# Optimization experiments

Hardware: AMD Instinct MI355X
Metric: run time of the kernel (lower is better)

The kernel has to match this reference:

```python
import jax, jax.numpy as jnp
import numpy as np

B, CIN, COUT, T, H, W, NH = 8, 16, 16, 32, 16, 16, 4
DIN = CIN * H * W    # 4096
DOUT = COUT * H * W  # 4096
DH = DOUT // NH      # 1024


def conv3d(x, w, b, pad):
    y = jax.lax.conv_general_dilated(
        x, w, window_strides=(1, 1, 1), padding=((pad, pad),) * 3,
        dimension_numbers=('NCDHW', 'OIDHW', 'NCDHW'))
    return y + b[None, :, None, None, None]


def instance_norm(x, eps=1e-5):
    # InstanceNorm3d default: no affine, normalize per (B,C) over (T,H,W)
    mu = x.mean(axis=(2, 3, 4), keepdims=True)
    var = ((x - mu) ** 2).mean(axis=(2, 3, 4), keepdims=True)
    return (x - mu) * jax.lax.rsqrt(var + eps)


def slstm(x, Wg, bg, Rg):
    # x: (B,T,D). Wg: (4,D,D) input weights [i,f,z,o]; bg: (4,D);
    # Rg: (NH,4,DH,DH) block-diagonal per-head recurrent weights.
    Bb, Tt, D = x.shape
    Gx = jnp.einsum('btd,god->btgo', x, Wg) + bg  # (B,T,4,D)

    def step(carry, gx):
        h, c, n, m = carry
        hh = h.reshape(Bb, NH, DH)
        gh = jnp.einsum('bhd,hgod->bhgo', hh, Rg)          # (B,NH,4,DH)
        pre = gx + gh.transpose(0, 2, 1, 3).reshape(Bb, 4, D)
        i_pre, f_pre, z_pre, o_pre = pre[:, 0], pre[:, 1], pre[:, 2], pre[:, 3]
        # stabilized exponential gating (xLSTM sLSTM)
        m_new = jnp.maximum(f_pre + m, i_pre)
        i = jnp.exp(i_pre - m_new)
        f = jnp.exp(f_pre + m - m_new)
        c = f * c + i * jnp.tanh(z_pre)
        n = f * n + i
        h = jax.nn.sigmoid(o_pre) * c / n
        return (h, c, n, m_new), h

    init = tuple(jnp.zeros((Bb, D), x.dtype) for _ in range(4))
    _, hs = jax.lax.scan(step, init, Gx.transpose(1, 0, 2, 3))  # hs: (T,B,D)
    return hs.transpose(1, 0, 2)


def setup_inputs():
    key = jax.random.key(0)
    ks = jax.random.split(key, 8)
    s = 0.02
    return {
        'x': jax.random.normal(ks[0], (B, CIN, T, H, W), jnp.float32),
        'c1_w': jax.random.normal(ks[1], (COUT, CIN, 3, 3, 3), jnp.float32) * 0.05,
        'c1_b': jnp.zeros((COUT,), jnp.float32),
        'c2_w': jax.random.normal(ks[2], (COUT, COUT, 3, 3, 3), jnp.float32) * 0.05,
        'c2_b': jnp.zeros((COUT,), jnp.float32),
        'c3_w': jax.random.normal(ks[3], (COUT, COUT, 3, 3, 3), jnp.float32) * 0.05,
        'c3_b': jnp.zeros((COUT,), jnp.float32),
        'pre_w': jax.random.normal(ks[4], (DOUT, DIN), jnp.float32) * s,
        'pre_b': jnp.zeros((DOUT,), jnp.float32),
        'lstm_W': jax.random.normal(ks[5], (4, DOUT, DOUT), jnp.float32) * s,
        'lstm_b': jnp.zeros((4, DOUT), jnp.float32),
        'lstm_R': jax.random.normal(ks[6], (NH, 4, DH, DH), jnp.float32) * s,
        'attn_w': jax.random.normal(ks[7], (1, 2 * COUT), jnp.float32) * 0.05,
        'attn_b': jnp.zeros((1,), jnp.float32),
    }


def reference(x, c1_w, c1_b, c2_w, c2_b, c3_w, c3_b, pre_w, pre_b,
              lstm_W, lstm_b, lstm_R, attn_w, attn_b):
    # conv3d branch: conv -> IN -> relu -> conv -> relu -> conv -> relu
    y = jax.nn.relu(instance_norm(conv3d(x, c1_w, c1_b, 1)))
    y = jax.nn.relu(conv3d(y, c2_w, c2_b, 1))
    out3d = jax.nn.relu(conv3d(y, c3_w, c3_b, 1))
    # sLSTM branch
    xs = x.transpose(0, 2, 1, 3, 4).reshape(B, T, DIN)
    xs = xs @ pre_w.T + pre_b
    hs = slstm(xs, lstm_W, lstm_b, lstm_R)                 # (B,T,DOUT)
    s_out = hs.reshape(B, T, COUT, H, W).transpose(0, 2, 1, 3, 4)
    # attention-gated fusion: cat -> 1x1x1 conv -> sigmoid -> weighted sum
    comb = jnp.concatenate([s_out, out3d], axis=1)         # (B,2*COUT,T,H,W)
    alpha = jax.nn.sigmoid(jnp.einsum('bcthw,oc->bothw', comb, attn_w)
                           + attn_b[None, :, None, None, None])
    return alpha * out3d + (1 - alpha) * s_out
```

## Files before the change

kernel.cpp:

```cpp
#include <hip/hip_runtime.h>
#include <hip/hip_bf16.h>
#include <cstddef>

#define BB   8
#define CIN  16
#define COUT 16
#define TT   32
#define HH   16
#define WW   16
#define DIN  4096
#define DOUT 4096
#define NH   4
#define DH   1024
#define SPAT 8192
#define NSEQ 256

typedef __attribute__((ext_vector_type(8))) short  bf16x8;
typedef __attribute__((ext_vector_type(4))) float  f32x4;
typedef __attribute__((ext_vector_type(4))) unsigned short us4;
typedef __attribute__((ext_vector_type(4))) int    i32x4;
typedef unsigned short ushort_t;
typedef unsigned long long u64_t;

static __device__ __forceinline__ ushort_t f2bf(float f) {
    union { float f; unsigned u; } v; v.f = f;
    unsigned r = (v.u + 0x7fffu + ((v.u >> 16) & 1u)) >> 16;
    return (ushort_t)r;
}
static __device__ __forceinline__ float bf2f(ushort_t u) {
    union { unsigned u; float f; } v; v.u = ((unsigned)u) << 16;
    return v.f;
}

__global__ void setup_kernel(const float* __restrict__ x, ushort_t* __restrict__ xt,
                             const float* __restrict__ w1, const float* __restrict__ w2,
                             const float* __restrict__ w3,
                             float* __restrict__ cw1, float* __restrict__ cw2,
                             float* __restrict__ cw3, int* __restrict__ flags) {
    int bid = blockIdx.x;
    if (bid < 1024) {
        int idx = bid * 256 + threadIdx.x;
        int n = idx >> 10, k4 = (idx & 1023) * 4;
        int b = n >> 5, t = n & 31, c = k4 >> 8, hw = k4 & 255;
        f32x4 f = *(const f32x4*)&x[(((size_t)(b * CIN + c) * TT + t)) * 256 + hw];
        us4 o;
        #pragma unroll
        for (int i = 0; i < 4; ++i) o[i] = f2bf(f[i]);
        *(us4*)&xt[(size_t)n * DIN + k4] = o;
    } else if (bid < 1105) {
        int i = (bid - 1024) * 256 + threadIdx.x;
        if (i < 3 * 6912) {
            int set = i / 6912, j = i - set * 6912;
            const float* w = (set == 0) ? w1 : (set == 1) ? w2 : w3;
            float* cw      = (set == 0) ? cw1 : (set == 1) ? cw2 : cw3;
            int o = j & 15, r = j >> 4;
            int k = r % 27, ci = r / 27;
            cw[j] = w[(size_t)(o * CIN + ci) * 27 + k];
        }
    } else {
        int j = (bid - 1105) * 256 + threadIdx.x;
        ((i32x4*)flags)[j] = (i32x4){0, 0, 0, 0};
    }
}

template<int BN, int BK, bool OUT_BF16, bool ADD_BIAS>
__device__ __forceinline__
void gemm_body(char* smem, int bx, int by, int nsplit,
               const ushort_t* __restrict__ A, const float* __restrict__ B,
               const float* __restrict__ bias, void* __restrict__ C,
               int N, int K) {
    constexpr int NF  = BN / 16;
    constexpr int TPR = 256 / BN;
    constexpr int FPT = BK / TPR;
    ushort_t* Al = (ushort_t*)smem;
    ushort_t* Bl = Al + 2 * 256 * BK;
    int tid  = threadIdx.x;
    int lane = tid & 63;
    int wv   = tid >> 6;
    int n0 = bx * BN;
    int ksp = K / nsplit;
    int kS  = by * ksp;

    f32x4 acc[4][NF];
    #pragma unroll
    for (int i = 0; i < 4; ++i)
        #pragma unroll
        for (int j = 0; j < NF; ++j) acc[i][j] = (f32x4){0.f, 0.f, 0.f, 0.f};

    auto stageA = [&](int buf, int k0) {
        #pragma unroll
        for (int q = 0; q < 8; ++q) {
            int rbase = wv * 64 + q * 8;
            int row = rbase + (lane >> 3);
            const ushort_t* g = A + (size_t)row * K + k0 + (lane & 7) * 8;
            __builtin_amdgcn_global_load_lds(
                (const __attribute__((address_space(1))) void*)g,
                (__attribute__((address_space(3))) void*)&Al[(buf * 256 + rbase) * BK],
                16, 0, 0);
        }
    };
    auto stageB = [&](int buf, int k0) {
        int r  = tid / TPR;
        int cs = (tid % TPR) * FPT;
        const float* g = B + (size_t)(n0 + r) * K + k0 + cs;
        #pragma unroll
        for (int q = 0; q < FPT / 4; ++q) {
            f32x4 f = *(const f32x4*)(g + q * 4);
            us4 pk;
            #pragma unroll
            for (int e = 0; e < 4; ++e) pk[e] = f2bf(f[e]);
            *(us4*)&Bl[(buf * BN + r) * BK + cs + q * 4] = pk;
        }
    };
    auto compute = [&](int buf) {
        #pragma unroll
        for (int ks = 0; ks < BK / 32; ++ks) {
            bf16x8 af[4], bfr[NF];
            #pragma unroll
            for (int i = 0; i < 4; ++i)
                af[i] = *(const bf16x8*)&Al[(buf * 256 + wv * 64 + i * 16 + (lane & 15)) * BK + ks * 32 + (lane >> 4) * 8];
            #pragma unroll
            for (int j = 0; j < NF; ++j)
                bfr[j] = *(const bf16x8*)&Bl[(buf * BN + j * 16 + (lane & 15)) * BK + ks * 32 + (lane >> 4) * 8];
            #pragma unroll
            for (int i = 0; i < 4; ++i)
                #pragma unroll
                for (int j = 0; j < NF; ++j)
                    acc[i][j] = __builtin_amdgcn_mfma_f32_16x16x32_bf16(af[i], bfr[j], acc[i][j], 0, 0, 0);
        }
    };

    stageA(0, kS); stageB(0, kS);
    __syncthreads();
    int nk = ksp / BK;
    int cur = 0;
    for (int t = 0; t < nk; ++t) {
        if (t + 1 < nk) { stageA(cur ^ 1, kS + (t + 1) * BK); stageB(cur ^ 1, kS + (t + 1) * BK); }
        compute(cur);
        __syncthreads();
        cur ^= 1;
    }

    size_t cofs = (size_t)by * 256 * N;
    #pragma unroll
    for (int i = 0; i < 4; ++i) {
        int row = wv * 64 + i * 16 + (lane >> 4) * 4;
        #pragma unroll
        for (int j = 0; j < NF; ++j) {
            int col = n0 + j * 16 + (lane & 15);
            float bv = ADD_BIAS ? bias[col] : 0.f;
            #pragma unroll
            for (int r = 0; r < 4; ++r) {
                float v = acc[i][j][r] + bv;
                if constexpr (OUT_BF16) ((ushort_t*)C)[cofs + (size_t)(row + r) * N + col] = f2bf(v);
                else                    ((float*)C)[cofs + (size_t)(row + r) * N + col] = v;
            }
        }
    }
}

template<bool NORM, bool PSUM>
__device__ __forceinline__
void conv_body(char* smem, int blk,
               const float* __restrict__ in, const float* __restrict__ cw,
               const float* __restrict__ bias, const float* __restrict__ stats,
               float* __restrict__ out, float* __restrict__ psum, int relu) {
    float* xin = (float*)smem;
    int b = blk >> 6, t = (blk >> 1) & 31, half = blk & 1;
    int tid = threadIdx.x;

    for (int i = tid; i < CIN * 3 * 256; i += 256) {
        int hw = i & 255, r = i >> 8;
        int kt = r % 3, ci = r / 3;
        int tt = t + kt - 1;
        float v = 0.f;
        if ((unsigned)tt < TT) {
            v = in[((size_t)(b * CIN + ci) * TT + tt) * 256 + hw];
            if constexpr (NORM) {
                float mu = stats[(b * CIN + ci) * 2];
                float rs = stats[(b * CIN + ci) * 2 + 1];
                v = fmaxf((v - mu) * rs, 0.f);
            }
        }
        xin[(ci * 3 + kt) * 256 + hw] = v;
    }
    __syncthreads();

    int h = tid >> 4, wx = tid & 15;
    f32x4 a0 = *(const f32x4*)&bias[half * 8];
    f32x4 a1 = *(const f32x4*)&bias[half * 8 + 4];

    for (int ci = 0; ci < CIN; ++ci) {
        #pragma unroll
        for (int kt = 0; kt < 3; ++kt) {
            #pragma unroll
            for (int kh = 0; kh < 3; ++kh) {
                int h2 = h + kh - 1;
                bool vh = (unsigned)h2 < HH;
                int h2c = vh ? h2 : 0;
                #pragma unroll
                for (int kw = 0; kw < 3; ++kw) {
                    int w2 = wx + kw - 1;
                    bool v = vh && ((unsigned)w2 < WW);
                    int w2c = ((unsigned)w2 < WW) ? w2 : 0;
                    float xv = xin[(ci * 3 + kt) * 256 + h2c * 16 + w2c];
                    xv = v ? xv : 0.f;
                    const float* wp = cw + (size_t)(ci * 27 + kt * 9 + kh * 3 + kw) * 16 + half * 8;
                    f32x4 w0 = *(const f32x4*)(wp);
                    f32x4 w1 = *(const f32x4*)(wp + 4);
                    a0 += xv * w0; a1 += xv * w1;
                }
            }
        }
    }
    float accs[8];
    #pragma unroll
    for (int i = 0; i < 4; ++i) { accs[i] = a0[i]; accs[4 + i] = a1[i]; }
    #pragma unroll
    for (int o = 0; o < 8; ++o) {
        float v = accs[o];
        if (relu) v = fmaxf(v, 0.f);
        out[((size_t)(b * COUT + half * 8 + o) * TT + t) * 256 + tid] = v;
    }

    if constexpr (PSUM) {
        __syncthreads();
        float* sm = xin;
        int wv = tid >> 6;
        #pragma unroll
        for (int o = 0; o < 8; ++o) {
            float s = accs[o];
            float q = accs[o] * accs[o];
            #pragma unroll
            for (int m = 1; m < 64; m <<= 1) {
                s += __shfl_xor(s, m, 64);
                q += __shfl_xor(q, m, 64);
            }
            if ((tid & 63) == 0) { sm[wv * 16 + o * 2] = s; sm[wv * 16 + o * 2 + 1] = q; }
        }
        __syncthreads();
        if (tid < 16) {
            int o = tid >> 1, which = tid & 1;
            float v = sm[o * 2 + which] + sm[16 + o * 2 + which]
                    + sm[32 + o * 2 + which] + sm[48 + o * 2 + which];
            psum[((((size_t)(b * 32 + t) * 2 + half) * 8 + o) * 2) + which] = v;
        }
    }
}

__global__ __launch_bounds__(256, 2)
void fused1_kernel(const ushort_t* __restrict__ xt, const float* __restrict__ pre_w,
                   const float* __restrict__ pre_b, ushort_t* __restrict__ xs2b,
                   const float* __restrict__ x, const float* __restrict__ cw1,
                   const float* __restrict__ c1_b, float* __restrict__ y1,
                   float* __restrict__ psum) {
    extern __shared__ char smem[];
    if (blockIdx.x < 256)
        gemm_body<16, 64, true, true>(smem, blockIdx.x, 0, 1, xt, pre_w, pre_b, xs2b, DOUT, DIN);
    else
        conv_body<false, true>(smem, blockIdx.x - 256, x, cw1, c1_b, nullptr, y1, psum, 0);
}

__global__ __launch_bounds__(256, 2)
void fused2_kernel(const ushort_t* __restrict__ xs2b, const float* __restrict__ lstm_W,
                   float* __restrict__ Gx,
                   const float* __restrict__ y1, const float* __restrict__ cw2,
                   const float* __restrict__ c2_b, const float* __restrict__ stats,
                   float* __restrict__ y2) {
    extern __shared__ char smem[];
    if (blockIdx.x < 1024)
        gemm_body<32, 64, false, false>(smem, blockIdx.x & 511, blockIdx.x >> 9, 2,
                                        xs2b, lstm_W, nullptr, Gx, 4 * DOUT, DOUT);
    else
        conv_body<true, false>(smem, blockIdx.x - 1024, y1, cw2, c2_b, stats, y2, nullptr, 1);
}

__global__ __launch_bounds__(256, 2)
void conv3_kernel(const float* __restrict__ y2, const float* __restrict__ cw3,
                  const float* __restrict__ c3_b, float* __restrict__ out3d) {
    extern __shared__ char smem[];
    conv_body<false, false>(smem, blockIdx.x, y2, cw3, c3_b, nullptr, out3d, nullptr, 1);
}

__global__ void inorm_stats_kernel(const float* __restrict__ psum, float* __restrict__ stats) {
    int tid = threadIdx.x;
    if (tid < 128) {
        int b = tid >> 4, c = tid & 15;
        int half = c >> 3, ch = c & 7;
        float sum = 0.f, sq = 0.f;
        for (int t = 0; t < TT; ++t) {
            size_t base = (((size_t)(b * 32 + t) * 2 + half) * 8 + ch) * 2;
            sum += psum[base];
            sq  += psum[base + 1];
        }
        float mu = sum / (float)SPAT;
        float var = sq / (float)SPAT - mu * mu;
        stats[(b * CIN + c) * 2]     = mu;
        stats[(b * CIN + c) * 2 + 1] = rsqrtf(var + 1e-5f);
    }
}

#define GXPS ((size_t)NSEQ * 4 * DOUT)

__global__ __launch_bounds__(256, 1)
void lstm_persist_kernel(const float* __restrict__ R,
                         const float* __restrict__ Gx,
                         const float* __restrict__ lstm_b,
                         unsigned* __restrict__ hfr,
                         int* __restrict__ flags) {
    __shared__ ushort_t Rl[4][32][64 * 8];
    __shared__ float gh_p[4][4][16][8];

    int tid  = threadIdx.x;
    int lane = tid & 63;
    int w    = tid >> 6;
    int head = blockIdx.x >> 6;
    int oc   = blockIdx.x & 63;

    #pragma unroll 4
    for (int n = 0; n < 64; ++n) {
        int g = n >> 4, r = n & 15;
        const float* src = R + ((size_t)((head * 4 + g) * DH + oc * 16 + r)) * DH + tid * 4;
        f32x4 f = *(const f32x4*)src;
        int k0 = tid * 4;
        int ks = k0 >> 5;
        int kI = (k0 >> 3) & 3;
        int e8 = k0 & 7;
        union { ushort_t u[4]; u64_t q; } pk;
        #pragma unroll
        for (int e = 0; e < 4; ++e) pk.u[e] = f2bf(f[e]);
        *(u64_t*)&Rl[g][ks][((kI << 4) | r) * 8 + e8] = pk.q;
    }

    int arow = lane & 15;
    int part = arow >> 3;
    int bb   = arow & 7;
    int kseg = lane >> 4;

    int gb  = tid >> 4;
    int gol = tid & 15;
    int gd  = head * DH + oc * 16 + gol;
    int o_h = oc * 16 + gol;
    unsigned hslot = ((unsigned)head * 32 + (o_h >> 5)) * 256 + gb * 32 + (o_h & 31);
    float c_r = 0.f, n_r = 0.f, m_r = 0.f;
    float lb0 = 0.f, lb1 = 0.f, lb2 = 0.f, lb3 = 0.f;
    if (tid < 128) {
        lb0 = lstm_b[gd];
        lb1 = lstm_b[DOUT + gd];
        lb2 = lstm_b[2 * DOUT + gd];
        lb3 = lstm_b[3 * DOUT + gd];
    }

    __syncthreads();

    for (int t = 0; t < TT; ++t) {
        float gx0 = lb0, gx1 = lb1, gx2 = lb2, gx3 = lb3;
        if (tid < 128) {
            size_t gxoff = ((size_t)(gb * TT + t)) * (4 * DOUT) + gd;
            #pragma unroll
            for (int p = 0; p < 2; ++p) {
                const float* gp = Gx + p * GXPS + gxoff;
                gx0 += gp[0];
                gx1 += gp[DOUT];
                gx2 += gp[2 * DOUT];
                gx3 += gp[3 * DOUT];
            }
        }

        if (t > 0) {
            const int* fl = flags + (((t - 1) * 4 + head) << 6);
            for (;;) {
                int v = __hip_atomic_load(fl + lane, __ATOMIC_RELAXED,
                                          __HIP_MEMORY_SCOPE_AGENT);
                if (__all(v != 0)) break;
                __builtin_amdgcn_s_sleep(1);
            }

            const u64_t* hb = (const u64_t*)hfr
                + ((((size_t)(t - 1) * 4 + head) * 32) * 256 + bb * 32 + kseg * 8) / 2;
            bf16x8 hf[8];
            #pragma unroll
            for (int j = 0; j < 8; ++j) {
                const u64_t* p = hb + (size_t)(w * 8 + j) * 128;
                union { ushort_t u[8]; bf16x8 v; } fr;
                #pragma unroll
                for (int e2 = 0; e2 < 4; ++e2) {
                    u64_t q = __hip_atomic_load(p + e2, __ATOMIC_RELAXED,
                                                __HIP_MEMORY_SCOPE_AGENT);
                    unsigned q0 = (unsigned)q, q1 = (unsigned)(q >> 32);
                    fr.u[e2 * 2]     = part ? (ushort_t)(q0 >> 16) : (ushort_t)(q0 & 0xffffu);
                    fr.u[e2 * 2 + 1] = part ? (ushort_t)(q1 >> 16) : (ushort_t)(q1 & 0xffffu);
                }
                hf[j] = fr.v;
            }

            f32x4 acc[4];
            #pragma unroll
            for (int g = 0; g < 4; ++g) acc[g] = (f32x4){0.f, 0.f, 0.f, 0.f};
            #pragma unroll
            for (int g = 0; g < 4; ++g)
                #pragma unroll
                for (int j = 0; j < 8; ++j) {
                    bf16x8 a = *(const bf16x8*)&Rl[g][w * 8 + j][lane * 8];
                    acc[g] = __builtin_amdgcn_mfma_f32_16x16x32_bf16(a, hf[j], acc[g], 0, 0, 0);
                }
            #pragma unroll
            for (int g = 0; g < 4; ++g)
                #pragma unroll
                for (int r = 0; r < 4; ++r)
                    acc[g][r] += __shfl_xor(acc[g][r], 8, 64);
            if (part == 0) {
                int orow0 = kseg * 4;
                #pragma unroll
                for (int g = 0; g < 4; ++g)
                    #pragma unroll
                    for (int r = 0; r < 4; ++r)
                        gh_p[w][g][orow0 + r][bb] = acc[g][r];
            }
        } else {
            for (int i = tid; i < 4 * 4 * 16 * 8; i += 256)
                ((float*)gh_p)[i] = 0.f;
        }
        __syncthreads();

        if (tid < 128) {
            float ip = gx0 +
                gh_p[0][0][gol][gb] + gh_p[1][0][gol][gb] + gh_p[2][0][gol][gb] + gh_p[3][0][gol][gb];
            float fp = gx1 +
                gh_p[0][1][gol][gb] + gh_p[1][1][gol][gb] + gh_p[2][1][gol][gb] + gh_p[3][1][gol][gb];
            float zp = gx2 +
                gh_p[0][2][gol][gb] + gh_p[1][2][gol][gb] + gh_p[2][2][gol][gb] + gh_p[3][2][gol][gb];
            float op = gx3 +
                gh_p[0][3][gol][gb] + gh_p[1][3][gol][gb] + gh_p[2][3][gol][gb] + gh_p[3][3][gol][gb];
            float mn = fmaxf(fp + m_r, ip);
            float iv = __expf(ip - mn);
            float fv = __expf(fp + m_r - mn);
            float zc = fminf(fmaxf(zp, -9.f), 9.f);
            float th = 1.f - 2.f / (__expf(2.f * zc) + 1.f);
            c_r = fv * c_r + iv * th;
            n_r = fv * n_r + iv;
            float sig = 1.f / (1.f + __expf(-op));
            float hv = sig * c_r / n_r;
            m_r = mn;
            unsigned hi = f2bf(hv);
            unsigned lo = f2bf(hv - bf2f((ushort_t)hi));
            __hip_atomic_store(&hfr[(size_t)t * 32768 + hslot],
                               hi | (lo << 16),
                               __ATOMIC_RELAXED, __HIP_MEMORY_SCOPE_AGENT);
        }
        __syncthreads();
        if (tid == 0)
            __hip_atomic_store(&flags[((t * 4 + head) << 6) + oc], 1,
                               __ATOMIC_RELAXED, __HIP_MEMORY_SCOPE_AGENT);
    }
}

__global__ void combine_kernel(const unsigned* __restrict__ hfr,
                               const float* __restrict__ out3d,
                               const float* __restrict__ attn_w,
                               const float* __restrict__ attn_b,
                               float* __restrict__ out) {
    int idx = blockIdx.x * 256 + threadIdx.x;
    int hw = idx & 255;
    int t  = (idx >> 8) & 31;
    int b  = idx >> 13;
    float dot = attn_b[0];
    float sv[16], ov[16];
    #pragma unroll
    for (int ch = 0; ch < 16; ++ch) {
        int d = ch * 256 + hw;
        int head = d >> 10, o_h = d & 1023;
        size_t slot = (size_t)t * 32768 + (size_t)head * 8192
                    + (o_h >> 5) * 256 + b * 32 + (o_h & 31);
        unsigned v32 = hfr[slot];
        float s = bf2f((ushort_t)(v32 & 0xffffu)) + bf2f((ushort_t)(v32 >> 16));
        float o3 = out3d[(((size_t)(b * COUT + ch) * TT + t)) * 256 + hw];
        sv[ch] = s; ov[ch] = o3;
        dot += attn_w[ch] * s + attn_w[16 + ch] * o3;
    }
    float alpha = 1.f / (1.f + expf(-dot));
    #pragma unroll
    for (int ch = 0; ch < 16; ++ch) {
        out[(((size_t)(b * COUT + ch) * TT + t)) * 256 + hw] =
            alpha * ov[ch] + (1.f - alpha) * sv[ch];
    }
}

extern "C" void kernel_launch(void* const* d_in, const int* in_sizes, int n_in,
                              void* d_out, int out_size, void* d_ws, size_t ws_size,
                              hipStream_t stream) {
    const float* x      = (const float*)d_in[0];
    const float* c1_w   = (const float*)d_in[1];
    const float* c1_b   = (const float*)d_in[2];
    const float* c2_w   = (const float*)d_in[3];
    const float* c2_b   = (const float*)d_in[4];
    const float* c3_w   = (const float*)d_in[5];
    const float* c3_b   = (const float*)d_in[6];
    const float* pre_w  = (const float*)d_in[7];
    const float* pre_b  = (const float*)d_in[8];
    const float* lstm_W = (const float*)d_in[9];
    const float* lstm_b = (const float*)d_in[10];
    const float* lstm_R = (const float*)d_in[11];
    const float* attn_w = (const float*)d_in[12];
    const float* attn_b = (const float*)d_in[13];
    float* out = (float*)d_out;

    float* wsf = (float*)d_ws;
    float* y1    = wsf;
    float* y2    = y1 + 1048576;
    float* out3d = y2 + 1048576;
    float* Gx    = out3d + 1048576;
    float* cw1   = Gx + 2 * 4194304;
    float* cw2   = cw1 + 6912;
    float* cw3   = cw2 + 6912;
    float* stats = cw3 + 6912;
    float* psum  = stats + 256;
    float* pad   = psum + 8192;
    ushort_t* xt   = (ushort_t*)(pad + 64);
    ushort_t* xs2b = xt + 1048576;
    unsigned* hfr  = (unsigned*)(xs2b + 1048576);
    int*     flags = (int*)(hfr + 1048576);

    setup_kernel<<<1113, 256, 0, stream>>>(x, xt, c1_w, c2_w, c3_w, cw1, cw2, cw3, flags);

    fused1_kernel<<<768, 256, 69632, stream>>>(xt, pre_w, pre_b, xs2b,
                                               x, cw1, c1_b, y1, psum);
    inorm_stats_kernel<<<1, 256, 0, stream>>>(psum, stats);

    fused2_kernel<<<1536, 256, 73728, stream>>>(xs2b, lstm_W, Gx,
                                                y1, cw2, c2_b, stats, y2);

    conv3_kernel<<<512, 256, 49152, stream>>>(y2, cw3, c3_b, out3d);

    lstm_persist_kernel<<<256, 256, 0, stream>>>(lstm_R, Gx, lstm_b, hfr, flags);

    combine_kernel<<<256, 256, 0, stream>>>(hfr, out3d, attn_w, attn_b, out);
}
```

Baseline: 531.4 us.

## Fuse instance-norm stats, conv3 and combine into neighbouring kernels via flags

```diff
diff --git a/kernel.cpp b/kernel.cpp
--- a/kernel.cpp
+++ b/kernel.cpp
@@ -59,7 +59,8 @@
         }
     } else {
         int j = (bid - 1105) * 256 + threadIdx.x;
-        ((i32x4*)flags)[j] = (i32x4){0, 0, 0, 0};
+        if (j < 2176)
+            ((i32x4*)flags)[j] = (i32x4){0, 0, 0, 0};
     }
 }
 
@@ -159,37 +160,12 @@
     }
 }
 
-template<bool NORM, bool PSUM>
 __device__ __forceinline__
-void conv_body(char* smem, int blk,
-               const float* __restrict__ in, const float* __restrict__ cw,
-               const float* __restrict__ bias, const float* __restrict__ stats,
-               float* __restrict__ out, float* __restrict__ psum, int relu) {
-    float* xin = (float*)smem;
-    int b = blk >> 6, t = (blk >> 1) & 31, half = blk & 1;
-    int tid = threadIdx.x;
-
-    for (int i = tid; i < CIN * 3 * 256; i += 256) {
-        int hw = i & 255, r = i >> 8;
-        int kt = r % 3, ci = r / 3;
-        int tt = t + kt - 1;
-        float v = 0.f;
-        if ((unsigned)tt < TT) {
-            v = in[((size_t)(b * CIN + ci) * TT + tt) * 256 + hw];
-            if constexpr (NORM) {
-                float mu = stats[(b * CIN + ci) * 2];
-                float rs = stats[(b * CIN + ci) * 2 + 1];
-                v = fmaxf((v - mu) * rs, 0.f);
-            }
-        }
-        xin[(ci * 3 + kt) * 256 + hw] = v;
-    }
-    __syncthreads();
-
+void conv_taps(const float* xin, const float* __restrict__ cw, int half,
+               const float* __restrict__ bias, float* accs, int tid) {
     int h = tid >> 4, wx = tid & 15;
     f32x4 a0 = *(const f32x4*)&bias[half * 8];
     f32x4 a1 = *(const f32x4*)&bias[half * 8 + 4];
-
     for (int ci = 0; ci < CIN; ++ci) {
         #pragma unroll
         for (int kt = 0; kt < 3; ++kt) {
@@ -213,39 +189,152 @@
             }
         }
     }
-    float accs[8];
     #pragma unroll
     for (int i = 0; i < 4; ++i) { accs[i] = a0[i]; accs[4 + i] = a1[i]; }
+}
+
+__device__ __forceinline__
+void conv1_body(char* smem, int blk,
+                const float* __restrict__ in, const float* __restrict__ cw,
+                const float* __restrict__ bias,
+                float* __restrict__ out, float* __restrict__ psum) {
+    float* xin = (float*)smem;
+    int b = blk >> 6, t = (blk >> 1) & 31, half = blk & 1;
+    int tid = threadIdx.x;
+
+    for (int i = tid; i < CIN * 3 * 256; i += 256) {
+        int hw = i & 255, r = i >> 8;
+        int kt = r % 3, ci = r / 3;
+        int tt = t + kt - 1;
+        float v = 0.f;
+        if ((unsigned)tt < TT)
+            v = in[((size_t)(b * CIN + ci) * TT + tt) * 256 + hw];
+        xin[(ci * 3 + kt) * 256 + hw] = v;
+    }
+    __syncthreads();
+
+    float accs[8];
+    conv_taps(xin, cw, half, bias, accs, tid);
+    #pragma unroll
+    for (int o = 0; o < 8; ++o)
+        out[((size_t)(b * COUT + half * 8 + o) * TT + t) * 256 + tid] = accs[o];
+
+    __syncthreads();
+    float* sm = xin;
+    int wv = tid >> 6;
     #pragma unroll
     for (int o = 0; o < 8; ++o) {
-        float v = accs[o];
-        if (relu) v = fmaxf(v, 0.f);
-        out[((size_t)(b * COUT + half * 8 + o) * TT + t) * 256 + tid] = v;
-    }
-
-    if constexpr (PSUM) {
-        __syncthreads();
-        float* sm = xin;
-        int wv = tid >> 6;
-        #pragma unroll
-        for (int o = 0; o < 8; ++o) {
-            float s = accs[o];
-            float q = accs[o] * accs[o];
-            #pragma unroll
-            for (int m = 1; m < 64; m <<= 1) {
-                s += __shfl_xor(s, m, 64);
-                q += __shfl_xor(q, m, 64);
+        float s = accs[o];
+        float q = accs[o] * accs[o];
+        #pragma unroll
+        for (int m = 1; m < 64; m <<= 1) {
+            s += __shfl_xor(s, m, 64);
+            q += __shfl_xor(q, m, 64);
+        }
+        if ((tid & 63) == 0) { sm[wv * 16 + o * 2] = s; sm[wv * 16 + o * 2 + 1] = q; }
+    }
+    __syncthreads();
+    if (tid < 16) {
+        int o = tid >> 1, which = tid & 1;
+        float v = sm[o * 2 + which] + sm[16 + o * 2 + which]
+                + sm[32 + o * 2 + which] + sm[48 + o * 2 + which];
+        psum[((((size_t)(b * 32 + t) * 2 + half) * 8 + o) * 2) + which] = v;
+    }
+}
+
+__device__ __forceinline__
+void conv2_body(char* smem, int blk,
+                const float* __restrict__ y1, const float* __restrict__ cw,
+                const float* __restrict__ bias, const float* __restrict__ psum,
+                float* __restrict__ y2, int* __restrict__ cflags) {
+    float* xin = (float*)smem;
+    float* sstats = xin + 12288;
+    int b = blk >> 6, t = (blk >> 1) & 31, half = blk & 1;
+    int tid = threadIdx.x;
+
+    if (tid < 16) {
+        int c = tid;
+        float sum = 0.f, sq = 0.f;
+        for (int t2 = 0; t2 < 32; ++t2) {
+            size_t base = (((size_t)(b * 32 + t2) * 2 + (c >> 3)) * 8 + (c & 7)) * 2;
+            sum += psum[base];
+            sq  += psum[base + 1];
+        }
+        float mu = sum / (float)SPAT;
+        float var = sq / (float)SPAT - mu * mu;
+        sstats[c * 2]     = mu;
+        sstats[c * 2 + 1] = rsqrtf(var + 1e-5f);
+    }
+    __syncthreads();
+
+    for (int i = tid; i < CIN * 3 * 256; i += 256) {
+        int hw = i & 255, r = i >> 8;
+        int kt = r % 3, ci = r / 3;
+        int tt = t + kt - 1;
+        float v = 0.f;
+        if ((unsigned)tt < TT) {
+            v = y1[((size_t)(b * CIN + ci) * TT + tt) * 256 + hw];
+            v = fmaxf((v - sstats[ci * 2]) * sstats[ci * 2 + 1], 0.f);
+        }
+        xin[(ci * 3 + kt) * 256 + hw] = v;
+    }
+    __syncthreads();
+
+    float accs[8];
+    conv_taps(xin, cw, half, bias, accs, tid);
+    #pragma unroll
+    for (int o = 0; o < 8; ++o) {
+        float v = fmaxf(accs[o], 0.f);
+        __hip_atomic_store(&y2[((size_t)(b * COUT + half * 8 + o) * TT + t) * 256 + tid],
+                           v, __ATOMIC_RELAXED, __HIP_MEMORY_SCOPE_AGENT);
+    }
+    __syncthreads();
+    if (tid == 0)
+        __hip_atomic_store(&cflags[blk], 1, __ATOMIC_RELAXED, __HIP_MEMORY_SCOPE_AGENT);
+}
+
+__device__ __forceinline__
+void conv3_body(char* smem, int blk,
+                const float* __restrict__ y2, const float* __restrict__ cw,
+                const float* __restrict__ bias, float* __restrict__ out3d,
+                const int* __restrict__ cflags) {
+    float* xin = (float*)smem;
+    int b = blk >> 6, t = (blk >> 1) & 31, half = blk & 1;
+    int tid = threadIdx.x;
+
+    if (tid == 0) {
+        #pragma unroll
+        for (int dt = -1; dt <= 1; ++dt) {
+            int tn = t + dt;
+            if ((unsigned)tn >= TT) continue;
+            #pragma unroll
+            for (int hh = 0; hh < 2; ++hh) {
+                const int* f = &cflags[(b << 6) | (tn << 1) | hh];
+                while (__hip_atomic_load(f, __ATOMIC_RELAXED,
+                                         __HIP_MEMORY_SCOPE_AGENT) == 0)
+                    __builtin_amdgcn_s_sleep(1);
             }
-            if ((tid & 63) == 0) { sm[wv * 16 + o * 2] = s; sm[wv * 16 + o * 2 + 1] = q; }
-        }
-        __syncthreads();
-        if (tid < 16) {
-            int o = tid >> 1, which = tid & 1;
-            float v = sm[o * 2 + which] + sm[16 + o * 2 + which]
-                    + sm[32 + o * 2 + which] + sm[48 + o * 2 + which];
-            psum[((((size_t)(b * 32 + t) * 2 + half) * 8 + o) * 2) + which] = v;
-        }
-    }
+        }
+    }
+    __syncthreads();
+
+    for (int i = tid; i < CIN * 3 * 256; i += 256) {
+        int hw = i & 255, r = i >> 8;
+        int kt = r % 3, ci = r / 3;
+        int tt = t + kt - 1;
+        float v = 0.f;
+        if ((unsigned)tt < TT)
+            v = __hip_atomic_load(&y2[((size_t)(b * CIN + ci) * TT + tt) * 256 + hw],
+                                  __ATOMIC_RELAXED, __HIP_MEMORY_SCOPE_AGENT);
+        xin[(ci * 3 + kt) * 256 + hw] = v;
+    }
+    __syncthreads();
+
+    float accs[8];
+    conv_taps(xin, cw, half, bias, accs, tid);
+    #pragma unroll
+    for (int o = 0; o < 8; ++o)
+        out3d[((size_t)(b * COUT + half * 8 + o) * TT + t) * 256 + tid] = fmaxf(accs[o], 0.f);
 }
 
 __global__ __launch_bounds__(256, 2)
@@ -258,46 +347,25 @@
     if (blockIdx.x < 256)
         gemm_body<16, 64, true, true>(smem, blockIdx.x, 0, 1, xt, pre_w, pre_b, xs2b, DOUT, DIN);
     else
-        conv_body<false, true>(smem, blockIdx.x - 256, x, cw1, c1_b, nullptr, y1, psum, 0);
+        conv1_body(smem, blockIdx.x - 256, x, cw1, c1_b, y1, psum);
 }
 
 __global__ __launch_bounds__(256, 2)
 void fused2_kernel(const ushort_t* __restrict__ xs2b, const float* __restrict__ lstm_W,
                    float* __restrict__ Gx,
                    const float* __restrict__ y1, const float* __restrict__ cw2,
-                   const float* __restrict__ c2_b, const float* __restrict__ stats,
-                   float* __restrict__ y2) {
+                   const float* __restrict__ c2_b, const float* __restrict__ psum,
+                   float* __restrict__ y2,
+                   const float* __restrict__ cw3, const float* __restrict__ c3_b,
+                   float* __restrict__ out3d, int* __restrict__ cflags) {
     extern __shared__ char smem[];
     if (blockIdx.x < 1024)
         gemm_body<32, 64, false, false>(smem, blockIdx.x & 511, blockIdx.x >> 9, 2,
                                         xs2b, lstm_W, nullptr, Gx, 4 * DOUT, DOUT);
+    else if (blockIdx.x < 1536)
+        conv2_body(smem, blockIdx.x - 1024, y1, cw2, c2_b, psum, y2, cflags);
     else
-        conv_body<true, false>(smem, blockIdx.x - 1024, y1, cw2, c2_b, stats, y2, nullptr, 1);
-}
-
-__global__ __launch_bounds__(256, 2)
-void conv3_kernel(const float* __restrict__ y2, const float* __restrict__ cw3,
-                  const float* __restrict__ c3_b, float* __restrict__ out3d) {
-    extern __shared__ char smem[];
-    conv_body<false, false>(smem, blockIdx.x, y2, cw3, c3_b, nullptr, out3d, nullptr, 1);
-}
-
-__global__ void inorm_stats_kernel(const float* __restrict__ psum, float* __restrict__ stats) {
-    int tid = threadIdx.x;
-    if (tid < 128) {
-        int b = tid >> 4, c = tid & 15;
-        int half = c >> 3, ch = c & 7;
-        float sum = 0.f, sq = 0.f;
-        for (int t = 0; t < TT; ++t) {
-            size_t base = (((size_t)(b * 32 + t) * 2 + half) * 8 + ch) * 2;
-            sum += psum[base];
-            sq  += psum[base + 1];
-        }
-        float mu = sum / (float)SPAT;
-        float var = sq / (float)SPAT - mu * mu;
-        stats[(b * CIN + c) * 2]     = mu;
-        stats[(b * CIN + c) * 2 + 1] = rsqrtf(var + 1e-5f);
-    }
+        conv3_body(smem, blockIdx.x - 1536, y2, cw3, c3_b, out3d, cflags);
 }
 
 #define GXPS ((size_t)NSEQ * 4 * DOUT)
@@ -307,7 +375,11 @@
                          const float* __restrict__ Gx,
                          const float* __restrict__ lstm_b,
                          unsigned* __restrict__ hfr,
-                         int* __restrict__ flags) {
+                         int* __restrict__ flags,
+                         const float* __restrict__ out3d,
+                         const float* __restrict__ attn_w,
+                         const float* __restrict__ attn_b,
+                         float* __restrict__ out) {
     __shared__ ushort_t Rl[4][32][64 * 8];
     __shared__ float gh_p[4][4][16][8];
 
@@ -453,36 +525,44 @@
             __hip_atomic_store(&flags[((t * 4 + head) << 6) + oc], 1,
                                __ATOMIC_RELAXED, __HIP_MEMORY_SCOPE_AGENT);
     }
-}
-
-__global__ void combine_kernel(const unsigned* __restrict__ hfr,
-                               const float* __restrict__ out3d,
-                               const float* __restrict__ attn_w,
-                               const float* __restrict__ attn_b,
-                               float* __restrict__ out) {
-    int idx = blockIdx.x * 256 + threadIdx.x;
-    int hw = idx & 255;
-    int t  = (idx >> 8) & 31;
-    int b  = idx >> 13;
-    float dot = attn_b[0];
-    float sv[16], ov[16];
-    #pragma unroll
-    for (int ch = 0; ch < 16; ++ch) {
-        int d = ch * 256 + hw;
-        int head = d >> 10, o_h = d & 1023;
-        size_t slot = (size_t)t * 32768 + (size_t)head * 8192
-                    + (o_h >> 5) * 256 + b * 32 + (o_h & 31);
-        unsigned v32 = hfr[slot];
-        float s = bf2f((ushort_t)(v32 & 0xffffu)) + bf2f((ushort_t)(v32 >> 16));
-        float o3 = out3d[(((size_t)(b * COUT + ch) * TT + t)) * 256 + hw];
-        sv[ch] = s; ov[ch] = o3;
-        dot += attn_w[ch] * s + attn_w[16 + ch] * o3;
-    }
-    float alpha = 1.f / (1.f + expf(-dot));
-    #pragma unroll
-    for (int ch = 0; ch < 16; ++ch) {
-        out[(((size_t)(b * COUT + ch) * TT + t)) * 256 + hw] =
-            alpha * ov[ch] + (1.f - alpha) * sv[ch];
+
+    {
+        const int* fl31 = flags + ((31 * 4) << 6);
+        for (;;) {
+            int ok = 1;
+            #pragma unroll
+            for (int q = 0; q < 4; ++q)
+                ok &= (__hip_atomic_load(fl31 + q * 64 + lane, __ATOMIC_RELAXED,
+                                         __HIP_MEMORY_SCOPE_AGENT) != 0);
+            if (__all(ok)) break;
+            __builtin_amdgcn_s_sleep(1);
+        }
+
+        int idx = blockIdx.x * 256 + tid;
+        int hw = idx & 255;
+        int tC = (idx >> 8) & 31;
+        int bC = idx >> 13;
+        float dot = attn_b[0];
+        float sv[16], ov[16];
+        #pragma unroll
+        for (int ch = 0; ch < 16; ++ch) {
+            int d = ch * 256 + hw;
+            int hd2 = d >> 10, o_h2 = d & 1023;
+            size_t slot = (size_t)tC * 32768 + (size_t)hd2 * 8192
+                        + (o_h2 >> 5) * 256 + bC * 32 + (o_h2 & 31);
+            unsigned v32 = __hip_atomic_load(&hfr[slot], __ATOMIC_RELAXED,
+                                             __HIP_MEMORY_SCOPE_AGENT);
+            float s = bf2f((ushort_t)(v32 & 0xffffu)) + bf2f((ushort_t)(v32 >> 16));
+            float o3 = out3d[(((size_t)(bC * COUT + ch) * TT + tC)) * 256 + hw];
+            sv[ch] = s; ov[ch] = o3;
+            dot += attn_w[ch] * s + attn_w[16 + ch] * o3;
+        }
+        float alpha = 1.f / (1.f + expf(-dot));
+        #pragma unroll
+        for (int ch = 0; ch < 16; ++ch) {
+            out[(((size_t)(bC * COUT + ch) * TT + tC)) * 256 + hw] =
+                alpha * ov[ch] + (1.f - alpha) * sv[ch];
+        }
     }
 }
 
@@ -513,26 +593,23 @@
     float* cw1   = Gx + 2 * 4194304;
     float* cw2   = cw1 + 6912;
     float* cw3   = cw2 + 6912;
-    float* stats = cw3 + 6912;
-    float* psum  = stats + 256;
+    float* psum  = cw3 + 6912;
     float* pad   = psum + 8192;
     ushort_t* xt   = (ushort_t*)(pad + 64);
     ushort_t* xs2b = xt + 1048576;
     unsigned* hfr  = (unsigned*)(xs2b + 1048576);
     int*     flags = (int*)(hfr + 1048576);
-
-    setup_kernel<<<1113, 256, 0, stream>>>(x, xt, c1_w, c2_w, c3_w, cw1, cw2, cw3, flags);
+    int*    cflags = flags + 8192;
+
+    setup_kernel<<<1114, 256, 0, stream>>>(x, xt, c1_w, c2_w, c3_w, cw1, cw2, cw3, flags);
 
     fused1_kernel<<<768, 256, 69632, stream>>>(xt, pre_w, pre_b, xs2b,
                                                x, cw1, c1_b, y1, psum);
-    inorm_stats_kernel<<<1, 256, 0, stream>>>(psum, stats);
-
-    fused2_kernel<<<1536, 256, 73728, stream>>>(xs2b, lstm_W, Gx,
-                                                y1, cw2, c2_b, stats, y2);
-
-    conv3_kernel<<<512, 256, 49152, stream>>>(y2, cw3, c3_b, out3d);
-
-    lstm_persist_kernel<<<256, 256, 0, stream>>>(lstm_R, Gx, lstm_b, hfr, flags);
-
-    combine_kernel<<<256, 256, 0, stream>>>(hfr, out3d, attn_w, attn_b, out);
-}
+
+    fused2_kernel<<<2048, 256, 73728, stream>>>(xs2b, lstm_W, Gx,
+                                                y1, cw2, c2_b, psum, y2,
+                                                cw3, c3_b, out3d, cflags);
+
+    lstm_persist_kernel<<<256, 256, 0, stream>>>(lstm_R, Gx, lstm_b, hfr, flags,
+                                                 out3d, attn_w, attn_b, out);
+}
```

Result: no change. 528.6 us (-0.5%).
